# Kernel optimization log

Measured on AMD Instinct MI355X. Metric: run time of the kernel, lower is better.

Reference implementation:

```python
import jax, jax.numpy as jnp
import numpy as np

B, H, S, D = 16, 12, 1024, 64  # batch, heads, seq, head_dim (dim=768, num_head=12)


def setup_inputs() -> dict:
    key = jax.random.key(0)
    ks = jax.random.split(key, 9)
    sc = 1.0 / np.sqrt(D)
    return {
        "x": jax.random.normal(ks[0], (B, H, S, D), dtype=jnp.float32),
        "Wq": jax.random.normal(ks[1], (D, D), dtype=jnp.float32) * sc,
        "bq": jax.random.normal(ks[2], (D,), dtype=jnp.float32) * 0.02,
        "Wk": jax.random.normal(ks[3], (D, D), dtype=jnp.float32) * sc,
        "bk": jax.random.normal(ks[4], (D,), dtype=jnp.float32) * 0.02,
        "Wv": jax.random.normal(ks[5], (D, D), dtype=jnp.float32) * sc,
        "bv": jax.random.normal(ks[6], (D,), dtype=jnp.float32) * 0.02,
        "Wo": jax.random.normal(ks[7], (D, D), dtype=jnp.float32) * sc,
        "bo": jax.random.normal(ks[8], (D,), dtype=jnp.float32) * 0.02,
    }


def reference(x, Wq, bq, Wk, bk, Wv, bv, Wo, bo):
    # torch Linear: y = x @ W^T + b, applied to last dim (head_dim)
    q = jnp.einsum("bhsd,ed->bhse", x, Wq) + bq
    k = jnp.einsum("bhsd,ed->bhse", x, Wk) + bk
    v = jnp.einsum("bhsd,ed->bhse", x, Wv) + bv
    scores = jnp.einsum("bhqd,bhkd->bhqk", q, k) / jnp.sqrt(jnp.float32(q.shape[-1]))
    attn = jax.nn.softmax(scores, axis=-1)
    out = jnp.einsum("bhqk,bhkd->bhqd", attn, v)
    out = jnp.einsum("bhsd,ed->bhse", out, Wo) + bo
    return out
```

## Files before the change

kernel.cpp:

```cpp
#include <hip/hip_runtime.h>
#include <math.h>


typedef __bf16 bf16x8 __attribute__((ext_vector_type(8)));
typedef float  f32x4  __attribute__((ext_vector_type(4)));

#define MFMA(a, b, c) __builtin_amdgcn_mfma_f32_16x16x32_bf16((a), (b), (c), 0, 0, 0)

static constexpr int S = 1024;
static constexpr int PAD = 72;
static constexpr size_t NE = 196608ull * 64ull;
static constexpr float QSCALE = 0.125f * 1.4426950408889634f;

__device__ inline unsigned long long pack4bf(float a, float b, float c, float d) {
    union { __bf16 h[4]; unsigned long long u; } pk;
    pk.h[0] = (__bf16)a; pk.h[1] = (__bf16)b; pk.h[2] = (__bf16)c; pk.h[3] = (__bf16)d;
    return pk.u;
}

union frag_u { bf16x8 v; unsigned long long u[2]; };

__global__ void w_conv(const float* __restrict__ Wq, const float* __restrict__ Wk,
                       const float* __restrict__ Wv, const float* __restrict__ Wo,
                       __bf16* __restrict__ wqb, __bf16* __restrict__ wkb,
                       __bf16* __restrict__ wvb, __bf16* __restrict__ wob)
{
    const int grp = blockIdx.x >> 2;
    const int p   = (((blockIdx.x & 3) * 256) + threadIdx.x) * 4;
    if (grp == 3) {
        int e = p >> 6, s = p & 63;
        int h = s >> 5, qp = (s >> 3) & 3, tb = (s >> 2) & 1;
        int d0 = 32 * h + 16 * tb + 4 * qp;
        float4 v = *(const float4*)(Wo + e * 64 + d0);
        *(unsigned long long*)(wob + p) = pack4bf(v.x, v.y, v.z, v.w);
    } else {
        const float* src = (grp == 0) ? Wq : (grp == 1) ? Wk : Wv;
        __bf16*      dst = (grp == 0) ? wqb : (grp == 1) ? wkb : wvb;
        float4 v = *(const float4*)(src + p);
        *(unsigned long long*)(dst + p) = pack4bf(v.x, v.y, v.z, v.w);
    }
}

__global__ __launch_bounds__(256, 4) void proj_qkv(
    const float* __restrict__ x,
    const __bf16* __restrict__ wqb, const __bf16* __restrict__ wkb,
    const __bf16* __restrict__ wvb,
    const float* __restrict__ bq, const float* __restrict__ bk,
    const float* __restrict__ bv,
    __bf16* __restrict__ gq, __bf16* __restrict__ gk, __bf16* __restrict__ gvt)
{
    __shared__ __align__(16) __bf16 lx[128][PAD];
    __shared__ __align__(16) __bf16 lbuf[128][PAD];

    const int tid = threadIdx.x;
    const int row_base = blockIdx.x * 128;

    #pragma unroll
    for (int i = tid * 4; i < 8192; i += 1024) {
        float4 v = *(const float4*)(x + (size_t)row_base * 64 + i);
        int r = i >> 6, c = i & 63;
        *(unsigned long long*)&lx[r][c] = pack4bf(v.x, v.y, v.z, v.w);
    }
    __syncthreads();

    const int w = tid >> 6, lane = tid & 63, m = lane & 15, quad = lane >> 4;
    const int bh = row_base >> 10;
    const int s_base = row_base & 1023;

    bf16x8 xf[2][2];
    #pragma unroll
    for (int g = 0; g < 2; g++) {
        xf[g][0] = *(const bf16x8*)&lx[w * 32 + g * 16 + m][quad * 8];
        xf[g][1] = *(const bf16x8*)&lx[w * 32 + g * 16 + m][32 + quad * 8];
    }

    #pragma unroll
    for (int mtx = 0; mtx < 2; mtx++) {
        const __bf16* wb = (mtx == 0) ? wqb : wkb;
        const float*  bb = (mtx == 0) ? bq  : bk;
        #pragma unroll
        for (int et = 0; et < 4; et++) {
            bf16x8 wf0 = *(const bf16x8*)(wb + (size_t)(et * 16 + m) * 64 + quad * 8);
            bf16x8 wf1 = *(const bf16x8*)(wb + (size_t)(et * 16 + m) * 64 + 32 + quad * 8);
            float4 bias = *(const float4*)(bb + et * 16 + quad * 4);
            #pragma unroll
            for (int g = 0; g < 2; g++) {
                f32x4 acc = {0.f, 0.f, 0.f, 0.f};
                acc = MFMA(wf0, xf[g][0], acc);
                acc = MFMA(wf1, xf[g][1], acc);
                unsigned long long u;
                if (mtx == 0)
                    u = pack4bf((acc[0] + bias.x) * QSCALE, (acc[1] + bias.y) * QSCALE,
                                (acc[2] + bias.z) * QSCALE, (acc[3] + bias.w) * QSCALE);
                else
                    u = pack4bf(acc[0] + bias.x, acc[1] + bias.y,
                                acc[2] + bias.z, acc[3] + bias.w);
                *(unsigned long long*)&lbuf[w * 32 + g * 16 + m][et * 16 + quad * 4] = u;
            }
        }
        __syncthreads();
        __bf16* dst = (mtx == 0 ? gq : gk);
        #pragma unroll
        for (int it = 0; it < 4; it++) {
            int idx = it * 256 + tid;
            int row = idx >> 3, col = (idx & 7) * 8;
            *(uint4*)(dst + ((size_t)row_base + row) * 64 + col) = *(uint4*)&lbuf[row][col];
        }
        __syncthreads();
    }

    __bf16 (*lvt)[136] = (__bf16(*)[136])&lbuf[0][0];
    #pragma unroll
    for (int et = 0; et < 4; et++) {
        bf16x8 wf0 = *(const bf16x8*)(wvb + (size_t)(et * 16 + m) * 64 + quad * 8);
        bf16x8 wf1 = *(const bf16x8*)(wvb + (size_t)(et * 16 + m) * 64 + 32 + quad * 8);
        const float bias = bv[et * 16 + m];
        #pragma unroll
        for (int g = 0; g < 2; g++) {
            f32x4 acc = {0.f, 0.f, 0.f, 0.f};
            acc = MFMA(xf[g][0], wf0, acc);
            acc = MFMA(xf[g][1], wf1, acc);
            const int tp = (2 * w + g) & 3;
            const int p0 = 64 * (w >> 1) + 32 * (tp >> 1) + 8 * quad + 4 * (tp & 1);
            *(unsigned long long*)&lvt[et * 16 + m][p0] =
                pack4bf(acc[0] + bias, acc[1] + bias, acc[2] + bias, acc[3] + bias);
        }
    }
    __syncthreads();
    #pragma unroll
    for (int it = 0; it < 4; it++) {
        int idx = it * 256 + tid;
        int row = idx >> 4, col = (idx & 15) * 8;
        *(uint4*)(gvt + ((size_t)bh * 64 + row) * 1024 + s_base + col) = *(uint4*)&lvt[row][col];
    }
}

__global__ __launch_bounds__(256) void attn(
    const __bf16* __restrict__ gq, const __bf16* __restrict__ gk,
    const __bf16* __restrict__ gvt, const __bf16* __restrict__ wob,
    const float* __restrict__ bo, float* __restrict__ out)
{
    __shared__ __align__(16) __bf16 lk[64][PAD];
    __shared__ __align__(16) __bf16 lv[64][PAD];

    const int tid = threadIdx.x;
    const int w = tid >> 6, lane = tid & 63, m = lane & 15, quad = lane >> 4;
    const int bh = blockIdx.x;
    const int q0 = blockIdx.y * 256 + w * 64;

    bf16x8 qf[4][2];
    #pragma unroll
    for (int g = 0; g < 4; g++) {
        const __bf16* qrow = gq + ((size_t)bh * S + q0 + g * 16 + m) * 64;
        qf[g][0] = *(const bf16x8*)(qrow + quad * 8);
        qf[g][1] = *(const bf16x8*)(qrow + 32 + quad * 8);
    }

    f32x4 o[4][4];
    float lsum[4] = {0.f, 0.f, 0.f, 0.f};
    #pragma unroll
    for (int g = 0; g < 4; g++)
        #pragma unroll
        for (int n = 0; n < 4; n++) o[g][n] = {0.f, 0.f, 0.f, 0.f};

    const int sr = tid >> 3;
    const int sc = (tid & 7) * 8;
    const __bf16* kbase = gk + (size_t)bh * S * 64;
    const __bf16* vbase = gvt + (size_t)bh * 64 * 1024;

    uint4 kreg0 = *(const uint4*)(kbase + (size_t)sr * 64 + sc);
    uint4 kreg1 = *(const uint4*)(kbase + (size_t)(sr + 32) * 64 + sc);
    uint4 vreg0 = *(const uint4*)(vbase + (size_t)sr * 1024 + sc);
    uint4 vreg1 = *(const uint4*)(vbase + (size_t)(sr + 32) * 1024 + sc);

    for (int kb = 0; kb < 16; kb++) {
        __syncthreads();
        *(uint4*)&lk[sr][sc]      = kreg0;
        *(uint4*)&lk[sr + 32][sc] = kreg1;
        *(uint4*)&lv[sr][sc]      = vreg0;
        *(uint4*)&lv[sr + 32][sc] = vreg1;
        if (kb < 15) {
            const int nb = (kb + 1) * 64;
            kreg0 = *(const uint4*)(kbase + (size_t)(nb + sr) * 64 + sc);
            kreg1 = *(const uint4*)(kbase + (size_t)(nb + sr + 32) * 64 + sc);
            vreg0 = *(const uint4*)(vbase + (size_t)sr * 1024 + nb + sc);
            vreg1 = *(const uint4*)(vbase + (size_t)(sr + 32) * 1024 + nb + sc);
        }
        __syncthreads();

        #pragma unroll
        for (int gp = 0; gp < 2; gp++) {
            frag_u pb[2][2];
            #pragma unroll
            for (int t = 0; t < 4; t++) {
                bf16x8 ka0 = *(const bf16x8*)&lk[t * 16 + m][quad * 8];
                bf16x8 ka1 = *(const bf16x8*)&lk[t * 16 + m][32 + quad * 8];
                #pragma unroll
                for (int gl = 0; gl < 2; gl++) {
                    const int g = gp * 2 + gl;
                    f32x4 acc = {0.f, 0.f, 0.f, 0.f};
                    acc = MFMA(ka0, qf[g][0], acc);
                    acc = MFMA(ka1, qf[g][1], acc);
                    float e0 = __builtin_amdgcn_exp2f(acc[0]);
                    float e1 = __builtin_amdgcn_exp2f(acc[1]);
                    float e2 = __builtin_amdgcn_exp2f(acc[2]);
                    float e3 = __builtin_amdgcn_exp2f(acc[3]);
                    lsum[g] += (e0 + e1) + (e2 + e3);
                    pb[gl][t >> 1].u[t & 1] = pack4bf(e0, e1, e2, e3);
                }
            }
            #pragma unroll
            for (int n = 0; n < 4; n++) {
                bf16x8 va0 = *(const bf16x8*)&lv[n * 16 + m][quad * 8];
                bf16x8 va1 = *(const bf16x8*)&lv[n * 16 + m][32 + quad * 8];
                #pragma unroll
                for (int gl = 0; gl < 2; gl++) {
                    const int g = gp * 2 + gl;
                    o[g][n] = MFMA(va0, pb[gl][0].v, o[g][n]);
                    o[g][n] = MFMA(va1, pb[gl][1].v, o[g][n]);
                }
            }
        }
    }

    #pragma unroll
    for (int g = 0; g < 4; g++) {
        lsum[g] += __shfl_xor(lsum[g], 16);
        lsum[g] += __shfl_xor(lsum[g], 32);
    }

    bf16x8 wf[4][2];
    #pragma unroll
    for (int et = 0; et < 4; et++) {
        wf[et][0] = *(const bf16x8*)(wob + (size_t)(et * 16 + m) * 64 + quad * 8);
        wf[et][1] = *(const bf16x8*)(wob + (size_t)(et * 16 + m) * 64 + 32 + quad * 8);
    }
    float biasr[4];
    #pragma unroll
    for (int et = 0; et < 4; et++) biasr[et] = bo[et * 16 + m];

    #pragma unroll
    for (int g = 0; g < 4; g++) {
        const float inv = 1.f / lsum[g];
        frag_u af0, af1;
        af0.u[0] = pack4bf(o[g][0][0] * inv, o[g][0][1] * inv, o[g][0][2] * inv, o[g][0][3] * inv);
        af0.u[1] = pack4bf(o[g][1][0] * inv, o[g][1][1] * inv, o[g][1][2] * inv, o[g][1][3] * inv);
        af1.u[0] = pack4bf(o[g][2][0] * inv, o[g][2][1] * inv, o[g][2][2] * inv, o[g][2][3] * inv);
        af1.u[1] = pack4bf(o[g][3][0] * inv, o[g][3][1] * inv, o[g][3][2] * inv, o[g][3][3] * inv);
        #pragma unroll
        for (int et = 0; et < 4; et++) {
            f32x4 acc = {0.f, 0.f, 0.f, 0.f};
            acc = MFMA(af0.v, wf[et][0], acc);
            acc = MFMA(af1.v, wf[et][1], acc);
            #pragma unroll
            for (int r = 0; r < 4; r++) {
                size_t row = (size_t)bh * S + q0 + g * 16 + quad * 4 + r;
                out[row * 64 + et * 16 + m] = acc[r] + biasr[et];
            }
        }
    }
}

extern "C" void kernel_launch(void* const* d_in, const int* in_sizes, int n_in,
                              void* d_out, int out_size, void* d_ws, size_t ws_size,
                              hipStream_t stream) {
    const float* x  = (const float*)d_in[0];
    const float* Wq = (const float*)d_in[1];
    const float* bq = (const float*)d_in[2];
    const float* Wk = (const float*)d_in[3];
    const float* bk = (const float*)d_in[4];
    const float* Wv = (const float*)d_in[5];
    const float* bv = (const float*)d_in[6];
    const float* Wo = (const float*)d_in[7];
    const float* bo = (const float*)d_in[8];
    float* out = (float*)d_out;

    __bf16* gq  = (__bf16*)d_ws;
    __bf16* gk  = gq + NE;
    __bf16* gvt = gk + NE;
    __bf16* wob = gvt + NE;
    __bf16* wqb = wob + 4096;
    __bf16* wkb = wqb + 4096;
    __bf16* wvb = wkb + 4096;

    w_conv<<<16, 256, 0, stream>>>(Wq, Wk, Wv, Wo, wqb, wkb, wvb, wob);
    proj_qkv<<<1536, 256, 0, stream>>>(x, wqb, wkb, wvb, bq, bk, bv, gq, gk, gvt);
    attn<<<dim3(192, 4), 256, 0, stream>>>(gq, gk, gvt, wob, bo, out);
}
```

Measured before the change: 197.0 us.

## Fuse QKV projection into attention kernel, recompute K/V per query block

The separate QKV projection kernel is removed. A prep kernel now converts x to bf16 alongside the weights. The attention kernel projects Q for its own rows, and inside the key loop projects K and V from bf16 x tiles held in shared memory. This cuts the global write and re-read of Q, K and V^T. In exchange, each of the four query blocks per head recomputes the K/V projections, adding MFMA work and extra barriers in the inner loop.

```diff
diff --git a/kernel.cpp b/kernel.cpp
--- a/kernel.cpp
+++ b/kernel.cpp
@@ -20,140 +20,114 @@
 
 union frag_u { bf16x8 v; unsigned long long u[2]; };
 
-__global__ void w_conv(const float* __restrict__ Wq, const float* __restrict__ Wk,
-                       const float* __restrict__ Wv, const float* __restrict__ Wo,
-                       __bf16* __restrict__ wqb, __bf16* __restrict__ wkb,
-                       __bf16* __restrict__ wvb, __bf16* __restrict__ wob)
+__global__ void prep(const float* __restrict__ x,
+                     const float* __restrict__ Wq, const float* __restrict__ Wk,
+                     const float* __restrict__ Wv, const float* __restrict__ Wo,
+                     __bf16* __restrict__ xb,
+                     __bf16* __restrict__ wqb, __bf16* __restrict__ wkb,
+                     __bf16* __restrict__ wvb, __bf16* __restrict__ wob)
 {
-    const int grp = blockIdx.x >> 2;
-    const int p   = (((blockIdx.x & 3) * 256) + threadIdx.x) * 4;
-    if (grp == 3) {
-        int e = p >> 6, s = p & 63;
-        int h = s >> 5, qp = (s >> 3) & 3, tb = (s >> 2) & 1;
-        int d0 = 32 * h + 16 * tb + 4 * qp;
-        float4 v = *(const float4*)(Wo + e * 64 + d0);
-        *(unsigned long long*)(wob + p) = pack4bf(v.x, v.y, v.z, v.w);
+    const int bid = blockIdx.x;
+    if (bid < 6144) {
+        size_t p = ((size_t)bid * 256 + threadIdx.x) * 8;
+        float4 a = *(const float4*)(x + p);
+        float4 b = *(const float4*)(x + p + 4);
+        union { unsigned long long u64[2]; uint4 v; } pk;
+        pk.u64[0] = pack4bf(a.x, a.y, a.z, a.w);
+        pk.u64[1] = pack4bf(b.x, b.y, b.z, b.w);
+        *(uint4*)(xb + p) = pk.v;
     } else {
-        const float* src = (grp == 0) ? Wq : (grp == 1) ? Wk : Wv;
-        __bf16*      dst = (grp == 0) ? wqb : (grp == 1) ? wkb : wvb;
-        float4 v = *(const float4*)(src + p);
-        *(unsigned long long*)(dst + p) = pack4bf(v.x, v.y, v.z, v.w);
-    }
-}
-
-__global__ __launch_bounds__(256, 4) void proj_qkv(
-    const float* __restrict__ x,
+        const int wb  = bid - 6144;
+        const int grp = wb >> 2;
+        const int p   = (((wb & 3) * 256) + threadIdx.x) * 4;
+        if (grp == 3) {
+            int e = p >> 6, s = p & 63;
+            int h = s >> 5, qp = (s >> 3) & 3, tb = (s >> 2) & 1;
+            int d0 = 32 * h + 16 * tb + 4 * qp;
+            float4 v = *(const float4*)(Wo + e * 64 + d0);
+            *(unsigned long long*)(wob + p) = pack4bf(v.x, v.y, v.z, v.w);
+        } else {
+            const float* src = (grp == 0) ? Wq : (grp == 1) ? Wk : Wv;
+            __bf16*      dst = (grp == 0) ? wqb : (grp == 1) ? wkb : wvb;
+            float4 v = *(const float4*)(src + p);
+            *(unsigned long long*)(dst + p) = pack4bf(v.x, v.y, v.z, v.w);
+        }
+    }
+}
+
+__global__ __launch_bounds__(256, 2) void attn(
+    const __bf16* __restrict__ xb,
     const __bf16* __restrict__ wqb, const __bf16* __restrict__ wkb,
-    const __bf16* __restrict__ wvb,
+    const __bf16* __restrict__ wvb, const __bf16* __restrict__ wob,
     const float* __restrict__ bq, const float* __restrict__ bk,
-    const float* __restrict__ bv,
-    __bf16* __restrict__ gq, __bf16* __restrict__ gk, __bf16* __restrict__ gvt)
+    const float* __restrict__ bv, const float* __restrict__ bo,
+    float* __restrict__ out)
 {
-    __shared__ __align__(16) __bf16 lx[128][PAD];
-    __shared__ __align__(16) __bf16 lbuf[128][PAD];
-
-    const int tid = threadIdx.x;
-    const int row_base = blockIdx.x * 128;
-
-    #pragma unroll
-    for (int i = tid * 4; i < 8192; i += 1024) {
-        float4 v = *(const float4*)(x + (size_t)row_base * 64 + i);
-        int r = i >> 6, c = i & 63;
-        *(unsigned long long*)&lx[r][c] = pack4bf(v.x, v.y, v.z, v.w);
-    }
-    __syncthreads();
-
-    const int w = tid >> 6, lane = tid & 63, m = lane & 15, quad = lane >> 4;
-    const int bh = row_base >> 10;
-    const int s_base = row_base & 1023;
-
-    bf16x8 xf[2][2];
-    #pragma unroll
-    for (int g = 0; g < 2; g++) {
-        xf[g][0] = *(const bf16x8*)&lx[w * 32 + g * 16 + m][quad * 8];
-        xf[g][1] = *(const bf16x8*)&lx[w * 32 + g * 16 + m][32 + quad * 8];
-    }
-
-    #pragma unroll
-    for (int mtx = 0; mtx < 2; mtx++) {
-        const __bf16* wb = (mtx == 0) ? wqb : wkb;
-        const float*  bb = (mtx == 0) ? bq  : bk;
-        #pragma unroll
-        for (int et = 0; et < 4; et++) {
-            bf16x8 wf0 = *(const bf16x8*)(wb + (size_t)(et * 16 + m) * 64 + quad * 8);
-            bf16x8 wf1 = *(const bf16x8*)(wb + (size_t)(et * 16 + m) * 64 + 32 + quad * 8);
-            float4 bias = *(const float4*)(bb + et * 16 + quad * 4);
-            #pragma unroll
-            for (int g = 0; g < 2; g++) {
-                f32x4 acc = {0.f, 0.f, 0.f, 0.f};
-                acc = MFMA(wf0, xf[g][0], acc);
-                acc = MFMA(wf1, xf[g][1], acc);
-                unsigned long long u;
-                if (mtx == 0)
-                    u = pack4bf((acc[0] + bias.x) * QSCALE, (acc[1] + bias.y) * QSCALE,
-                                (acc[2] + bias.z) * QSCALE, (acc[3] + bias.w) * QSCALE);
-                else
-                    u = pack4bf(acc[0] + bias.x, acc[1] + bias.y,
-                                acc[2] + bias.z, acc[3] + bias.w);
-                *(unsigned long long*)&lbuf[w * 32 + g * 16 + m][et * 16 + quad * 4] = u;
-            }
-        }
-        __syncthreads();
-        __bf16* dst = (mtx == 0 ? gq : gk);
-        #pragma unroll
-        for (int it = 0; it < 4; it++) {
-            int idx = it * 256 + tid;
-            int row = idx >> 3, col = (idx & 7) * 8;
-            *(uint4*)(dst + ((size_t)row_base + row) * 64 + col) = *(uint4*)&lbuf[row][col];
-        }
-        __syncthreads();
-    }
-
-    __bf16 (*lvt)[136] = (__bf16(*)[136])&lbuf[0][0];
-    #pragma unroll
-    for (int et = 0; et < 4; et++) {
-        bf16x8 wf0 = *(const bf16x8*)(wvb + (size_t)(et * 16 + m) * 64 + quad * 8);
-        bf16x8 wf1 = *(const bf16x8*)(wvb + (size_t)(et * 16 + m) * 64 + 32 + quad * 8);
-        const float bias = bv[et * 16 + m];
-        #pragma unroll
-        for (int g = 0; g < 2; g++) {
-            f32x4 acc = {0.f, 0.f, 0.f, 0.f};
-            acc = MFMA(xf[g][0], wf0, acc);
-            acc = MFMA(xf[g][1], wf1, acc);
-            const int tp = (2 * w + g) & 3;
-            const int p0 = 64 * (w >> 1) + 32 * (tp >> 1) + 8 * quad + 4 * (tp & 1);
-            *(unsigned long long*)&lvt[et * 16 + m][p0] =
-                pack4bf(acc[0] + bias, acc[1] + bias, acc[2] + bias, acc[3] + bias);
-        }
-    }
-    __syncthreads();
-    #pragma unroll
-    for (int it = 0; it < 4; it++) {
-        int idx = it * 256 + tid;
-        int row = idx >> 4, col = (idx & 15) * 8;
-        *(uint4*)(gvt + ((size_t)bh * 64 + row) * 1024 + s_base + col) = *(uint4*)&lvt[row][col];
-    }
-}
-
-__global__ __launch_bounds__(256) void attn(
-    const __bf16* __restrict__ gq, const __bf16* __restrict__ gk,
-    const __bf16* __restrict__ gvt, const __bf16* __restrict__ wob,
-    const float* __restrict__ bo, float* __restrict__ out)
-{
-    __shared__ __align__(16) __bf16 lk[64][PAD];
-    __shared__ __align__(16) __bf16 lv[64][PAD];
+    __shared__ __align__(16) union {
+        __bf16 xq[256][PAD];
+        struct {
+            __bf16 w[2][64][PAD];
+            __bf16 k[64][PAD];
+            __bf16 v[64][PAD];
+            __bf16 xk[64][PAD];
+        } m;
+    } L;
 
     const int tid = threadIdx.x;
     const int w = tid >> 6, lane = tid & 63, m = lane & 15, quad = lane >> 4;
     const int bh = blockIdx.x;
     const int q0 = blockIdx.y * 256 + w * 64;
 
+    const __bf16* xqbase = xb + ((size_t)bh * 1024 + blockIdx.y * 256) * 64;
+    #pragma unroll
+    for (int i = tid * 8, it = 0; it < 8; i += 2048, it++) {
+        int r = i >> 6, c = i & 63;
+        *(uint4*)&L.xq[r][c] = *(const uint4*)(xqbase + i);
+    }
+    __syncthreads();
+    bf16x8 xqf[4][2];
+    #pragma unroll
+    for (int g = 0; g < 4; g++) {
+        xqf[g][0] = *(const bf16x8*)&L.xq[w * 64 + g * 16 + m][quad * 8];
+        xqf[g][1] = *(const bf16x8*)&L.xq[w * 64 + g * 16 + m][32 + quad * 8];
+    }
+    __syncthreads();
+    #pragma unroll
+    for (int et = 0; et < 4; et++) {
+        bf16x8 wf0 = *(const bf16x8*)(wqb + (size_t)(et * 16 + m) * 64 + quad * 8);
+        bf16x8 wf1 = *(const bf16x8*)(wqb + (size_t)(et * 16 + m) * 64 + 32 + quad * 8);
+        float4 bias = *(const float4*)(bq + et * 16 + quad * 4);
+        #pragma unroll
+        for (int g = 0; g < 4; g++) {
+            f32x4 acc = {0.f, 0.f, 0.f, 0.f};
+            acc = MFMA(wf0, xqf[g][0], acc);
+            acc = MFMA(wf1, xqf[g][1], acc);
+            *(unsigned long long*)&L.xq[w * 64 + g * 16 + m][et * 16 + quad * 4] =
+                pack4bf((acc[0] + bias.x) * QSCALE, (acc[1] + bias.y) * QSCALE,
+                        (acc[2] + bias.z) * QSCALE, (acc[3] + bias.w) * QSCALE);
+        }
+    }
+    __syncthreads();
     bf16x8 qf[4][2];
     #pragma unroll
     for (int g = 0; g < 4; g++) {
-        const __bf16* qrow = gq + ((size_t)bh * S + q0 + g * 16 + m) * 64;
-        qf[g][0] = *(const bf16x8*)(qrow + quad * 8);
-        qf[g][1] = *(const bf16x8*)(qrow + 32 + quad * 8);
+        qf[g][0] = *(const bf16x8*)&L.xq[w * 64 + g * 16 + m][quad * 8];
+        qf[g][1] = *(const bf16x8*)&L.xq[w * 64 + g * 16 + m][32 + quad * 8];
+    }
+    __syncthreads();
+
+    #pragma unroll
+    for (int i = tid * 8, it = 0; it < 2; i += 2048, it++) {
+        int r = i >> 6, c = i & 63;
+        *(uint4*)&L.m.w[0][r][c] = *(const uint4*)(wkb + i);
+        *(uint4*)&L.m.w[1][r][c] = *(const uint4*)(wvb + i);
+    }
+    float4 bkr[4];
+    float  bvr[4];
+    #pragma unroll
+    for (int et = 0; et < 4; et++) {
+        bkr[et] = *(const float4*)(bk + et * 16 + quad * 4);
+        bvr[et] = bv[et * 16 + m];
     }
 
     f32x4 o[4][4];
@@ -163,38 +137,57 @@
         #pragma unroll
         for (int n = 0; n < 4; n++) o[g][n] = {0.f, 0.f, 0.f, 0.f};
 
-    const int sr = tid >> 3;
-    const int sc = (tid & 7) * 8;
-    const __bf16* kbase = gk + (size_t)bh * S * 64;
-    const __bf16* vbase = gvt + (size_t)bh * 64 * 1024;
-
-    uint4 kreg0 = *(const uint4*)(kbase + (size_t)sr * 64 + sc);
-    uint4 kreg1 = *(const uint4*)(kbase + (size_t)(sr + 32) * 64 + sc);
-    uint4 vreg0 = *(const uint4*)(vbase + (size_t)sr * 1024 + sc);
-    uint4 vreg1 = *(const uint4*)(vbase + (size_t)(sr + 32) * 1024 + sc);
+    const __bf16* xkey = xb + (size_t)bh * 1024 * 64;
+    uint4 px0 = *(const uint4*)(xkey + tid * 8);
+    uint4 px1 = *(const uint4*)(xkey + 2048 + tid * 8);
+
+    const int p0 = 32 * (w >> 1) + 8 * quad + 4 * (w & 1);
 
     for (int kb = 0; kb < 16; kb++) {
         __syncthreads();
-        *(uint4*)&lk[sr][sc]      = kreg0;
-        *(uint4*)&lk[sr + 32][sc] = kreg1;
-        *(uint4*)&lv[sr][sc]      = vreg0;
-        *(uint4*)&lv[sr + 32][sc] = vreg1;
+        {
+            int i0 = tid * 8;
+            int i1 = i0 + 2048;
+            *(uint4*)&L.m.xk[i0 >> 6][i0 & 63] = px0;
+            *(uint4*)&L.m.xk[i1 >> 6][i1 & 63] = px1;
+        }
+        __syncthreads();
+        {
+            bf16x8 xk0 = *(const bf16x8*)&L.m.xk[w * 16 + m][quad * 8];
+            bf16x8 xk1 = *(const bf16x8*)&L.m.xk[w * 16 + m][32 + quad * 8];
+            #pragma unroll
+            for (int et = 0; et < 4; et++) {
+                bf16x8 kw0 = *(const bf16x8*)&L.m.w[0][et * 16 + m][quad * 8];
+                bf16x8 kw1 = *(const bf16x8*)&L.m.w[0][et * 16 + m][32 + quad * 8];
+                f32x4 ka = {0.f, 0.f, 0.f, 0.f};
+                ka = MFMA(kw0, xk0, ka);
+                ka = MFMA(kw1, xk1, ka);
+                *(unsigned long long*)&L.m.k[w * 16 + m][et * 16 + quad * 4] =
+                    pack4bf(ka[0] + bkr[et].x, ka[1] + bkr[et].y,
+                            ka[2] + bkr[et].z, ka[3] + bkr[et].w);
+                bf16x8 vw0 = *(const bf16x8*)&L.m.w[1][et * 16 + m][quad * 8];
+                bf16x8 vw1 = *(const bf16x8*)&L.m.w[1][et * 16 + m][32 + quad * 8];
+                f32x4 va = {0.f, 0.f, 0.f, 0.f};
+                va = MFMA(xk0, vw0, va);
+                va = MFMA(xk1, vw1, va);
+                *(unsigned long long*)&L.m.v[et * 16 + m][p0] =
+                    pack4bf(va[0] + bvr[et], va[1] + bvr[et],
+                            va[2] + bvr[et], va[3] + bvr[et]);
+            }
+        }
         if (kb < 15) {
-            const int nb = (kb + 1) * 64;
-            kreg0 = *(const uint4*)(kbase + (size_t)(nb + sr) * 64 + sc);
-            kreg1 = *(const uint4*)(kbase + (size_t)(nb + sr + 32) * 64 + sc);
-            vreg0 = *(const uint4*)(vbase + (size_t)sr * 1024 + nb + sc);
-            vreg1 = *(const uint4*)(vbase + (size_t)(sr + 32) * 1024 + nb + sc);
+            const __bf16* xn = xkey + (kb + 1) * 4096;
+            px0 = *(const uint4*)(xn + tid * 8);
+            px1 = *(const uint4*)(xn + 2048 + tid * 8);
         }
         __syncthreads();
-
         #pragma unroll
         for (int gp = 0; gp < 2; gp++) {
             frag_u pb[2][2];
             #pragma unroll
             for (int t = 0; t < 4; t++) {
-                bf16x8 ka0 = *(const bf16x8*)&lk[t * 16 + m][quad * 8];
-                bf16x8 ka1 = *(const bf16x8*)&lk[t * 16 + m][32 + quad * 8];
+                bf16x8 ka0 = *(const bf16x8*)&L.m.k[t * 16 + m][quad * 8];
+                bf16x8 ka1 = *(const bf16x8*)&L.m.k[t * 16 + m][32 + quad * 8];
                 #pragma unroll
                 for (int gl = 0; gl < 2; gl++) {
                     const int g = gp * 2 + gl;
@@ -211,8 +204,8 @@
             }
             #pragma unroll
             for (int n = 0; n < 4; n++) {
-                bf16x8 va0 = *(const bf16x8*)&lv[n * 16 + m][quad * 8];
-                bf16x8 va1 = *(const bf16x8*)&lv[n * 16 + m][32 + quad * 8];
+                bf16x8 va0 = *(const bf16x8*)&L.m.v[n * 16 + m][quad * 8];
+                bf16x8 va1 = *(const bf16x8*)&L.m.v[n * 16 + m][32 + quad * 8];
                 #pragma unroll
                 for (int gl = 0; gl < 2; gl++) {
                     const int g = gp * 2 + gl;
@@ -275,15 +268,13 @@
     const float* bo = (const float*)d_in[8];
     float* out = (float*)d_out;
 
-    __bf16* gq  = (__bf16*)d_ws;
-    __bf16* gk  = gq + NE;
-    __bf16* gvt = gk + NE;
-    __bf16* wob = gvt + NE;
+    __bf16* xb  = (__bf16*)d_ws;
+    __bf16* wob = xb + NE;
     __bf16* wqb = wob + 4096;
     __bf16* wkb = wqb + 4096;
     __bf16* wvb = wkb + 4096;
 
-    w_conv<<<16, 256, 0, stream>>>(Wq, Wk, Wv, Wo, wqb, wkb, wvb, wob);
-    proj_qkv<<<1536, 256, 0, stream>>>(x, wqb, wkb, wvb, bq, bk, bv, gq, gk, gvt);
-    attn<<<dim3(192, 4), 256, 0, stream>>>(gq, gk, gvt, wob, bo, out);
-}
+    prep<<<6160, 256, 0, stream>>>(x, Wq, Wk, Wv, Wo, xb, wqb, wkb, wvb, wob);
+    attn<<<dim3(192, 4), 256, 0, stream>>>(xb, wqb, wkb, wvb, wob,
+                                           bq, bk, bv, bo, out);
+}
```

Result: no change. 195.9 us (-0.6%).
